# Optimization experiments

Hardware: AMD Instinct MI355X
Metric: run time of the kernel (lower is better)

The kernel has to match this reference:

```python
import jax, jax.numpy as jnp
import numpy as np

DIM = 32
DEPTH = 2  # closed-form Lyndon-basis log-signature implemented for depth 2


def setup_inputs() -> dict:
    key = jax.random.key(0)
    B, L, D = 512, 2048, DIM
    x = jax.random.normal(key, (B, L, D), dtype=jnp.float32)
    return {"x": x}


def _logsig_depth2(x):
    # x: (B, L, D) batch of paths.
    dx = x[:, 1:, :] - x[:, :-1, :]                     # (B, L-1, D) increments
    prefix = jnp.cumsum(dx, axis=1)                      # inclusive prefix sums
    level1 = prefix[:, -1, :]                            # (B, D) total displacement
    prefix_excl = prefix - dx                            # prefix up to t-1 (exclusive)
    # level-2 signature S_ij = sum_t prefix_excl[t, i] * dx[t, j]  -> (B, D, D)
    S2 = jnp.einsum("bli,blj->bij", prefix_excl, dx)
    # log-signature level 2 = antisymmetric part (Levy areas), Lyndon words i<j
    A = 0.5 * (S2 - jnp.swapaxes(S2, 1, 2))             # (B, D, D)
    iu, ju = jnp.triu_indices(x.shape[-1], k=1)          # row-major upper triangle
    areas = A[:, iu, ju]                                 # (B, D*(D-1)/2)
    return jnp.concatenate([level1, areas], axis=-1)     # (B, D + D*(D-1)/2)


def reference(x):
    # Faithful batched equivalent of iisignature.logsig(path, prepare(dim, 2))
    # for every path in the batch (Lyndon basis, depth 2).
    return _logsig_depth2(x)
```

## Files before the change

kernel.cpp:

```cpp
#include <hip/hip_runtime.h>
#include <stdint.h>


constexpr int kB   = 512;
constexpr int kL   = 2048;
constexpr int kD   = 32;
constexpr int kOut = 528;
constexpr int kPan = 32;
constexpr int kTw  = 512;
constexpr int kNP  = kTw / kPan;
constexpr int kCh  = 264;
constexpr int kPB  = 4 * kCh;

typedef __attribute__((ext_vector_type(8))) short bfrag;
typedef __attribute__((ext_vector_type(4))) float f4acc;
typedef __attribute__((ext_vector_type(4))) uint32_t u32x4;
union FragU { uint32_t u[4]; bfrag f; };

__global__ __launch_bounds__(256, 2)
void logsig_mfma(const float* __restrict__ x, float* __restrict__ out) {
    __shared__ __align__(16) uint32_t sStage[4][2][kPB];
    __shared__ float sx0[kD], sL1[kD];

    const int b    = blockIdx.x;
    const int tid  = threadIdx.x;
    const int wave = tid >> 6;
    const int lane = tid & 63;
    const int m    = lane & 15;
    const int q    = lane >> 4;

    const float* __restrict__ xb = x + (size_t)b * (kL * kD);
    const int t0w  = wave * kTw;
    const int grow = lane >> 3;
    const int gcol = (lane & 7) * 4;

    auto issue_g = [&](int p, u32x4 (&g)[4]) {
        const int rbase = t0w + p * kPan;
        #pragma unroll
        for (int c = 0; c < 4; ++c) {
            const uint32_t* gp = (const uint32_t*)xb
                               + (size_t)(rbase + c * 8 + grow) * kD + gcol;
            g[c] = *(const u32x4*)gp;
        }
    };
    auto write_g = [&](const u32x4 (&g)[4], int buf) {
        uint32_t* dst = &sStage[wave][buf][0];
        #pragma unroll
        for (int c = 0; c < 4; ++c)
            *(u32x4*)(dst + c * kCh + lane * 4) = g[c];
    };
    auto issue_h = [&](int p, uint32_t& h0, uint32_t& h1) {
        int hr = t0w + p * kPan + q * 8 + 8;
        hr = hr < kL - 1 ? hr : kL - 1;
        const uint32_t* gp = (const uint32_t*)xb + (size_t)hr * kD;
        h0 = gp[m];
        h1 = gp[m + 16];
    };

    f4acc acc[4];
    #pragma unroll
    for (int t = 0; t < 4; ++t)
        #pragma unroll
        for (int e = 0; e < 4; ++e) acc[t][e] = 0.0f;

    auto make_frags = [&](const uint32_t* e, FragU& AH, FragU& AL,
                          FragU& BH, FragU& BL) {
        uint32_t l[9];
        #pragma unroll
        for (int j = 0; j < 9; ++j) {
            const uint32_t fh = e[j] & 0xffff0000u;
            const float r = __builtin_bit_cast(float, e[j])
                          - __builtin_bit_cast(float, fh);
            l[j] = __builtin_bit_cast(uint32_t, r);
        }
        #pragma unroll
        for (int d = 0; d < 4; ++d) {
            AH.u[d] = __builtin_amdgcn_perm(e[2*d+1], e[2*d],   0x07060302u);
            AL.u[d] = __builtin_amdgcn_perm(l[2*d+1], l[2*d],   0x07060302u);
            BH.u[d] = __builtin_amdgcn_perm(e[2*d+2], e[2*d+1], 0x07060302u);
            BL.u[d] = __builtin_amdgcn_perm(l[2*d+2], l[2*d+1], 0x07060302u);
        }
    };

    u32x4 g[4], g2[4], g3[4];
    issue_g(0, g);
    write_g(g, 0);
    issue_g(1, g);
    issue_g(2, g2);

    #pragma unroll
    for (int p = 0; p < kNP; ++p) {
        const int cu = p & 1, nb = cu ^ 1;

        uint32_t h0, h1;
        issue_h(p, h0, h1);
        if (p + 3 < kNP) issue_g(p + 3, g3);

        const uint32_t* sb = &sStage[wave][cu][0];
        uint32_t e0[9], e1[9];
        #pragma unroll
        for (int j = 0; j < 8; ++j) {
            const int a = q * kCh + j * 32 + m;
            e0[j] = sb[a];
            e1[j] = sb[a + 16];
        }

        if (p + 1 < kNP) write_g(g, nb);
        if (p + 2 < kNP) {
            #pragma unroll
            for (int c = 0; c < 4; ++c) g[c] = g2[c];
        }
        if (p + 3 < kNP) {
            #pragma unroll
            for (int c = 0; c < 4; ++c) g2[c] = g3[c];
        }

        e0[8] = h0;
        e1[8] = h1;

        FragU A0H, A0L, B0H, B0L, A1H, A1L, B1H, B1L;
        make_frags(e0, A0H, A0L, B0H, B0L);
        make_frags(e1, A1H, A1L, B1H, B1L);

        acc[0] = __builtin_amdgcn_mfma_f32_16x16x32_bf16(A0H.f, B0H.f, acc[0], 0, 0, 0);
        acc[0] = __builtin_amdgcn_mfma_f32_16x16x32_bf16(A0H.f, B0L.f, acc[0], 0, 0, 0);
        acc[0] = __builtin_amdgcn_mfma_f32_16x16x32_bf16(A0L.f, B0H.f, acc[0], 0, 0, 0);
        acc[1] = __builtin_amdgcn_mfma_f32_16x16x32_bf16(A0H.f, B1H.f, acc[1], 0, 0, 0);
        acc[1] = __builtin_amdgcn_mfma_f32_16x16x32_bf16(A0H.f, B1L.f, acc[1], 0, 0, 0);
        acc[1] = __builtin_amdgcn_mfma_f32_16x16x32_bf16(A0L.f, B1H.f, acc[1], 0, 0, 0);
        acc[2] = __builtin_amdgcn_mfma_f32_16x16x32_bf16(A1H.f, B0H.f, acc[2], 0, 0, 0);
        acc[2] = __builtin_amdgcn_mfma_f32_16x16x32_bf16(A1H.f, B0L.f, acc[2], 0, 0, 0);
        acc[2] = __builtin_amdgcn_mfma_f32_16x16x32_bf16(A1L.f, B0H.f, acc[2], 0, 0, 0);
        acc[3] = __builtin_amdgcn_mfma_f32_16x16x32_bf16(A1H.f, B1H.f, acc[3], 0, 0, 0);
        acc[3] = __builtin_amdgcn_mfma_f32_16x16x32_bf16(A1H.f, B1L.f, acc[3], 0, 0, 0);
        acc[3] = __builtin_amdgcn_mfma_f32_16x16x32_bf16(A1L.f, B1H.f, acc[3], 0, 0, 0);
    }

    float* sWw = (float*)&sStage[wave][0][0];
    #pragma unroll
    for (int t = 0; t < 4; ++t) {
        const int tr = t >> 1, tc = t & 1;
        #pragma unroll
        for (int e = 0; e < 4; ++e) {
            const int row = 16 * tr + q * 4 + e;
            const int col = 16 * tc + m;
            sWw[row * kD + col] = acc[t][e];
        }
    }
    if (tid < kD) {
        const float x0v = xb[tid];
        const float xev = xb[(size_t)(kL - 1) * kD + tid];
        sx0[tid] = x0v;
        sL1[tid] = xev - x0v;
    }
    __syncthreads();

    float* sW0 = (float*)&sStage[0][0][0];
    for (int c = tid; c < kD * kD; c += 256)
        sW0[c] += ((float*)&sStage[1][0][0])[c]
                + ((float*)&sStage[2][0][0])[c]
                + ((float*)&sStage[3][0][0])[c];
    __syncthreads();

    float* ob = out + (size_t)b * kOut;
    for (int o = tid; o < kOut; o += 256) {
        if (o < 32) {
            ob[o] = sL1[o];
        } else {
            int p = o - 32, i = 0;
            while (p >= 31 - i) { p -= 31 - i; ++i; }
            const int j = i + 1 + p;
            float v = 0.5f * (sW0[i * kD + j] - sW0[j * kD + i])
                    + 0.5f * (sx0[j] * sL1[i] - sx0[i] * sL1[j]);
            ob[o] = v;
        }
    }
}

extern "C" void kernel_launch(void* const* d_in, const int* in_sizes, int n_in,
                              void* d_out, int out_size, void* d_ws, size_t ws_size,
                              hipStream_t stream) {
    const float* x = (const float*)d_in[0];
    float* out = (float*)d_out;
    logsig_mfma<<<dim3(kB), dim3(256), 0, stream>>>(x, out);
}
```

Measured before the change: 191.2 us.

## Load panels directly from global into registers and double waves per block

```diff
diff --git a/kernel.cpp b/kernel.cpp
--- a/kernel.cpp
+++ b/kernel.cpp
@@ -7,19 +7,16 @@
 constexpr int kD   = 32;
 constexpr int kOut = 528;
 constexpr int kPan = 32;
-constexpr int kTw  = 512;
+constexpr int kTw  = 256;
 constexpr int kNP  = kTw / kPan;
-constexpr int kCh  = 264;
-constexpr int kPB  = 4 * kCh;
 
 typedef __attribute__((ext_vector_type(8))) short bfrag;
 typedef __attribute__((ext_vector_type(4))) float f4acc;
-typedef __attribute__((ext_vector_type(4))) uint32_t u32x4;
 union FragU { uint32_t u[4]; bfrag f; };
 
-__global__ __launch_bounds__(256, 2)
+__global__ __launch_bounds__(512, 4)
 void logsig_mfma(const float* __restrict__ x, float* __restrict__ out) {
-    __shared__ __align__(16) uint32_t sStage[4][2][kPB];
+    __shared__ float sM[8][kD * kD];
     __shared__ float sx0[kD], sL1[kD];
 
     const int b    = blockIdx.x;
@@ -30,31 +27,22 @@
     const int q    = lane >> 4;
 
     const float* __restrict__ xb = x + (size_t)b * (kL * kD);
-    const int t0w  = wave * kTw;
-    const int grow = lane >> 3;
-    const int gcol = (lane & 7) * 4;
+    const uint32_t* __restrict__ xu = (const uint32_t*)xb;
+    const int t0w = wave * kTw;
 
-    auto issue_g = [&](int p, u32x4 (&g)[4]) {
-        const int rbase = t0w + p * kPan;
+    auto load_panel = [&](int p, uint32_t (&e0)[9], uint32_t (&e1)[9]) {
+        const int r0 = t0w + p * kPan + q * 8;
+        const uint32_t* gp = xu + (size_t)r0 * kD + m;
         #pragma unroll
-        for (int c = 0; c < 4; ++c) {
-            const uint32_t* gp = (const uint32_t*)xb
-                               + (size_t)(rbase + c * 8 + grow) * kD + gcol;
-            g[c] = *(const u32x4*)gp;
+        for (int j = 0; j < 8; ++j) {
+            e0[j] = gp[j * kD];
+            e1[j] = gp[j * kD + 16];
         }
-    };
-    auto write_g = [&](const u32x4 (&g)[4], int buf) {
-        uint32_t* dst = &sStage[wave][buf][0];
-        #pragma unroll
-        for (int c = 0; c < 4; ++c)
-            *(u32x4*)(dst + c * kCh + lane * 4) = g[c];
-    };
-    auto issue_h = [&](int p, uint32_t& h0, uint32_t& h1) {
-        int hr = t0w + p * kPan + q * 8 + 8;
+        int hr = r0 + 8;
         hr = hr < kL - 1 ? hr : kL - 1;
-        const uint32_t* gp = (const uint32_t*)xb + (size_t)hr * kD;
-        h0 = gp[m];
-        h1 = gp[m + 16];
+        const uint32_t* hp = xu + (size_t)hr * kD + m;
+        e0[8] = hp[0];
+        e1[8] = hp[16];
     };
 
     f4acc acc[4];
@@ -82,45 +70,21 @@
         }
     };
 
-    u32x4 g[4], g2[4], g3[4];
-    issue_g(0, g);
-    write_g(g, 0);
-    issue_g(1, g);
-    issue_g(2, g2);
+    uint32_t eA0[9], eA1[9], eB0[9], eB1[9];
+    load_panel(0, eA0, eA1);
 
     #pragma unroll
     for (int p = 0; p < kNP; ++p) {
-        const int cu = p & 1, nb = cu ^ 1;
+        const bool even = (p & 1) == 0;
+        auto& c0 = even ? eA0 : eB0;
+        auto& c1 = even ? eA1 : eB1;
+        auto& n0 = even ? eB0 : eA0;
+        auto& n1 = even ? eB1 : eA1;
 
-        uint32_t h0, h1;
-        issue_h(p, h0, h1);
-        if (p + 3 < kNP) issue_g(p + 3, g3);
-
-        const uint32_t* sb = &sStage[wave][cu][0];
-        uint32_t e0[9], e1[9];
-        #pragma unroll
-        for (int j = 0; j < 8; ++j) {
-            const int a = q * kCh + j * 32 + m;
-            e0[j] = sb[a];
-            e1[j] = sb[a + 16];
-        }
-
-        if (p + 1 < kNP) write_g(g, nb);
-        if (p + 2 < kNP) {
-            #pragma unroll
-            for (int c = 0; c < 4; ++c) g[c] = g2[c];
-        }
-        if (p + 3 < kNP) {
-            #pragma unroll
-            for (int c = 0; c < 4; ++c) g2[c] = g3[c];
-        }
-
-        e0[8] = h0;
-        e1[8] = h1;
-
+        if (p + 1 < kNP) load_panel(p + 1, n0, n1);
         FragU A0H, A0L, B0H, B0L, A1H, A1L, B1H, B1L;
-        make_frags(e0, A0H, A0L, B0H, B0L);
-        make_frags(e1, A1H, A1L, B1H, B1L);
+        make_frags(c0, A0H, A0L, B0H, B0L);
+        make_frags(c1, A1H, A1L, B1H, B1L);
 
         acc[0] = __builtin_amdgcn_mfma_f32_16x16x32_bf16(A0H.f, B0H.f, acc[0], 0, 0, 0);
         acc[0] = __builtin_amdgcn_mfma_f32_16x16x32_bf16(A0H.f, B0L.f, acc[0], 0, 0, 0);
@@ -136,7 +100,7 @@
         acc[3] = __builtin_amdgcn_mfma_f32_16x16x32_bf16(A1L.f, B1H.f, acc[3], 0, 0, 0);
     }
 
-    float* sWw = (float*)&sStage[wave][0][0];
+    float* sWw = sM[wave];
     #pragma unroll
     for (int t = 0; t < 4; ++t) {
         const int tr = t >> 1, tc = t & 1;
@@ -155,22 +119,23 @@
     }
     __syncthreads();
 
-    float* sW0 = (float*)&sStage[0][0][0];
-    for (int c = tid; c < kD * kD; c += 256)
-        sW0[c] += ((float*)&sStage[1][0][0])[c]
-                + ((float*)&sStage[2][0][0])[c]
-                + ((float*)&sStage[3][0][0])[c];
+    for (int c = tid; c < kD * kD; c += 512) {
+        float s = sM[0][c];
+        #pragma unroll
+        for (int w = 1; w < 8; ++w) s += sM[w][c];
+        sM[0][c] = s;
+    }
     __syncthreads();
 
     float* ob = out + (size_t)b * kOut;
-    for (int o = tid; o < kOut; o += 256) {
+    for (int o = tid; o < kOut; o += 512) {
         if (o < 32) {
             ob[o] = sL1[o];
         } else {
             int p = o - 32, i = 0;
             while (p >= 31 - i) { p -= 31 - i; ++i; }
             const int j = i + 1 + p;
-            float v = 0.5f * (sW0[i * kD + j] - sW0[j * kD + i])
+            float v = 0.5f * (sM[0][i * kD + j] - sM[0][j * kD + i])
                     + 0.5f * (sx0[j] * sL1[i] - sx0[i] * sL1[j]);
             ob[o] = v;
         }
@@ -182,5 +147,5 @@
                               hipStream_t stream) {
     const float* x = (const float*)d_in[0];
     float* out = (float*)d_out;
-    logsig_mfma<<<dim3(kB), dim3(256), 0, stream>>>(x, out);
+    logsig_mfma<<<dim3(kB), dim3(512), 0, stream>>>(x, out);
 }
```

Measured after the change: 188.5 us. No clear change (-1.4%).
